# Optimization experiments

Hardware: AMD Instinct MI355X
Metric: run time of the kernel (lower is better)

Reference implementation:

```python
import jax, jax.numpy as jnp
import numpy as np

N_NODES = 100000
N_EDGES = 3200000
D_IN = 256
D_OUT = 128
LN_EPS = 1e-5


def setup_inputs() -> dict:
    key = jax.random.key(0)
    ks = jax.random.split(key, 6)
    stdv = 1.0 / np.sqrt(D_OUT)
    x = jax.random.normal(ks[0], (N_NODES, D_IN), dtype=jnp.float32)
    weight = jax.random.uniform(ks[1], (D_IN, D_OUT), minval=-stdv, maxval=stdv, dtype=jnp.float32)
    bias = jnp.zeros((D_OUT,), dtype=jnp.float32)
    res_w = jax.random.normal(ks[2], (D_IN, D_OUT), dtype=jnp.float32) * 0.05
    res_b = jnp.zeros((D_OUT,), dtype=jnp.float32)
    ln_gamma = jnp.ones((D_OUT,), dtype=jnp.float32)
    ln_beta = jnp.zeros((D_OUT,), dtype=jnp.float32)
    edge_weight = jax.random.uniform(ks[3], (N_EDGES,), dtype=jnp.float32)
    edge_index = jax.random.randint(ks[4], (2, N_EDGES), 0, N_NODES, dtype=jnp.int32)
    return {"x": x, "weight": weight, "bias": bias, "res_w": res_w, "res_b": res_b,
            "ln_gamma": ln_gamma, "ln_beta": ln_beta,
            "edge_weight": edge_weight, "edge_index": edge_index}


def reference(x, weight, bias, res_w, res_b, ln_gamma, ln_beta, edge_weight, edge_index):
    # dense projection: [N, D_IN] @ [D_IN, D_OUT]
    support = x @ weight
    # spmm: out[dst] += w_e * support[src]  (weighted COO aggregation)
    src, dst = edge_index[0], edge_index[1]
    msg = support[src] * edge_weight[:, None]          # [E, D_OUT]
    out = jax.ops.segment_sum(msg, dst, num_segments=N_NODES)
    # fused bias + activated residual branch
    out = out + bias + jax.nn.relu(x @ res_w + res_b)
    # layernorm over feature dim
    mu = jnp.mean(out, axis=-1, keepdims=True)
    var = jnp.mean(jnp.square(out - mu), axis=-1, keepdims=True)
    out = (out - mu) * jax.lax.rsqrt(var + LN_EPS) * ln_gamma + ln_beta
    return out
```

## Files before the change

### kernel.cpp

```cpp
#include <hip/hip_runtime.h>
#include <hip/hip_bf16.h>

#define D_IN 256
#define D_OUT 128
#define LN_EPS 1e-5f
#define NBUCK 256
#define NCHUNK 256

typedef short bf16x8 __attribute__((ext_vector_type(8)));
typedef float f32x4 __attribute__((ext_vector_type(4)));
typedef unsigned short ushort_t;

__device__ __forceinline__ float b2f(ushort_t u) {
    union { unsigned int i; float f; } v; v.i = (unsigned int)u << 16; return v.f;
}
__device__ __forceinline__ ushort_t f2b(float f) {
    __hip_bfloat16 h = __float2bfloat16(f);
    return *reinterpret_cast<ushort_t*>(&h);
}

__global__ void k_transpose(const float* __restrict__ w, const float* __restrict__ rw,
                            ushort_t* __restrict__ wt) {
    int idx = blockIdx.x * 256 + threadIdx.x;
    int n = idx >> 8, k = idx & 255;
    float v = (n < 128) ? w[k * 128 + n] : rw[k * 128 + (n - 128)];
    wt[idx] = f2b(v);
}

__launch_bounds__(256)
__global__ void k_gemm(const float* __restrict__ x, const ushort_t* __restrict__ wt,
                       const float* __restrict__ bias, const float* __restrict__ res_b,
                       ushort_t* __restrict__ support, float* __restrict__ out, int n_nodes) {
    __shared__ ushort_t As[64 * 40];
    __shared__ ushort_t Bs[256 * 40];

    const int tid = threadIdx.x;
    const int m0 = blockIdx.x * 64;
    const int wv = tid >> 6, lane = tid & 63;
    const int lm = lane & 15, quad = lane >> 4;
    const int mh = wv >> 1;
    const int nh = wv & 1;

    f32x4 acc[2][8];
#pragma unroll
    for (int i = 0; i < 2; i++)
#pragma unroll
        for (int j = 0; j < 8; j++) acc[i][j] = 0.0f;

    const int arow = tid >> 2, aseg = tid & 3;
    const bool arow_ok = (m0 + arow) < n_nodes;
    const float* xrow = x + (long)(m0 + arow) * D_IN + aseg * 8;

    for (int kc = 0; kc < 8; kc++) {
        __syncthreads();
        {
            bf16x8 av = {0, 0, 0, 0, 0, 0, 0, 0};
            if (arow_ok) {
                f32x4 p0 = *(const f32x4*)(xrow + kc * 32);
                f32x4 p1 = *(const f32x4*)(xrow + kc * 32 + 4);
#pragma unroll
                for (int j = 0; j < 4; j++) { av[j] = (short)f2b(p0[j]); av[4 + j] = (short)f2b(p1[j]); }
            }
            *(bf16x8*)(&As[arow * 40 + aseg * 8]) = av;
        }
#pragma unroll
        for (int i = 0; i < 4; i++) {
            int n = (tid >> 2) + i * 64;
            bf16x8 v = *(const bf16x8*)(wt + n * 256 + kc * 32 + aseg * 8);
            *(bf16x8*)(&Bs[n * 40 + aseg * 8]) = v;
        }
        __syncthreads();

        bf16x8 afr0 = *(const bf16x8*)(&As[(mh * 32 + lm) * 40 + quad * 8]);
        bf16x8 afr1 = *(const bf16x8*)(&As[(mh * 32 + 16 + lm) * 40 + quad * 8]);
#pragma unroll
        for (int nt = 0; nt < 8; nt++) {
            bf16x8 bfr = *(const bf16x8*)(&Bs[(nh * 128 + nt * 16 + lm) * 40 + quad * 8]);
            acc[0][nt] = __builtin_amdgcn_mfma_f32_16x16x32_bf16(afr0, bfr, acc[0][nt], 0, 0, 0);
            acc[1][nt] = __builtin_amdgcn_mfma_f32_16x16x32_bf16(afr1, bfr, acc[1][nt], 0, 0, 0);
        }
    }

#pragma unroll
    for (int i = 0; i < 2; i++) {
#pragma unroll
        for (int nt = 0; nt < 8; nt++) {
            int col = nh * 128 + nt * 16 + lm;
#pragma unroll
            for (int r = 0; r < 4; r++) {
                int node = m0 + mh * 32 + i * 16 + quad * 4 + r;
                if (node >= n_nodes) continue;
                float v = acc[i][nt][r];
                if (col < 128) {
                    support[(long)node * 128 + col] = f2b(v);
                } else {
                    int c2 = col - 128;
                    float t = v + res_b[c2];
                    t = t > 0.0f ? t : 0.0f;
                    out[(long)node * 128 + c2] = t + bias[c2];
                }
            }
        }
    }
}

__launch_bounds__(256)
__global__ void k_count(const int* __restrict__ ei, int* __restrict__ cntmat, int E, int chunk) {
    __shared__ int h[NBUCK];
    int c = blockIdx.x, t = threadIdx.x;
    h[t] = 0;
    __syncthreads();
    int lo = c * chunk, hi = min(lo + chunk, E);
    for (int e = lo + t; e < hi; e += 256)
        atomicAdd(&h[(unsigned)ei[E + e] >> 9], 1);
    __syncthreads();
    cntmat[t * NCHUNK + c] = h[t];
}

__launch_bounds__(256)
__global__ void k_scan1(int* __restrict__ cntmat, int* __restrict__ rowsum) {
    __shared__ int sh[256];
    int b = blockIdx.x, t = threadIdx.x;
    int v = cntmat[b * NCHUNK + t];
    sh[t] = v;
    __syncthreads();
    for (int off = 1; off < 256; off <<= 1) {
        int x = sh[t]; int add = (t >= off) ? sh[t - off] : 0;
        __syncthreads(); sh[t] = x + add; __syncthreads();
    }
    cntmat[b * NCHUNK + t] = sh[t] - v;
    if (t == 255) rowsum[b] = sh[255];
}

__launch_bounds__(256)
__global__ void k_scan2(const int* __restrict__ rowsum, int* __restrict__ bucket_base,
                        int* __restrict__ offs, int n_nodes, int E) {
    __shared__ int sh[256];
    int t = threadIdx.x;
    int v = rowsum[t];
    sh[t] = v;
    __syncthreads();
    for (int off = 1; off < 256; off <<= 1) {
        int x = sh[t]; int add = (t >= off) ? sh[t - off] : 0;
        __syncthreads(); sh[t] = x + add; __syncthreads();
    }
    bucket_base[t] = sh[t] - v;
    if (t == 255) bucket_base[256] = sh[255];
    if (t == 0) offs[n_nodes] = E;
}

__launch_bounds__(256)
__global__ void k_part(const int* __restrict__ ei, const float* __restrict__ ew,
                       const int* __restrict__ cntmat, const int* __restrict__ bucket_base,
                       int* __restrict__ pk, ushort_t* __restrict__ pw, int E, int chunk) {
    __shared__ int cur[NBUCK];
    int c = blockIdx.x, t = threadIdx.x;
    cur[t] = bucket_base[t] + cntmat[t * NCHUNK + c];
    __syncthreads();
    int lo = c * chunk, hi = min(lo + chunk, E);
    for (int e = lo + t; e < hi; e += 256) {
        int src = ei[e];
        int dst = ei[E + e];
        float w = ew[e];
        int b = (unsigned)dst >> 9;
        int pos = atomicAdd(&cur[b], 1);
        pk[pos] = src | ((dst & 511) << 17);
        pw[pos] = f2b(w);
    }
}

__launch_bounds__(256)
__global__ void k_build(const int* __restrict__ pk, const ushort_t* __restrict__ pw,
                        const int* __restrict__ bucket_base, int* __restrict__ sk,
                        ushort_t* __restrict__ sw, int* __restrict__ offs, int n_nodes) {
    __shared__ int h[512];
    __shared__ int psum[256];
    int b = blockIdx.x, t = threadIdx.x;
    int start = bucket_base[b], end = bucket_base[b + 1];
    h[t] = 0; h[t + 256] = 0;
    __syncthreads();
    for (int i = start + t; i < end; i += 256)
        atomicAdd(&h[(unsigned)pk[i] >> 17], 1);
    __syncthreads();
    int h0 = h[2 * t], h1 = h[2 * t + 1];
    int p = h0 + h1;
    psum[t] = p;
    __syncthreads();
    for (int off = 1; off < 256; off <<= 1) {
        int x = psum[t]; int add = (t >= off) ? psum[t - off] : 0;
        __syncthreads(); psum[t] = x + add; __syncthreads();
    }
    int e0 = psum[t] - p;
    int e1 = e0 + h0;
    h[2 * t] = e0; h[2 * t + 1] = e1;
    int node0 = b * 512 + 2 * t;
    if (node0 < n_nodes) offs[node0] = start + e0;
    if (node0 + 1 < n_nodes) offs[node0 + 1] = start + e1;
    __syncthreads();
    for (int i = start + t; i < end; i += 256) {
        int key = pk[i];
        int dl = (unsigned)key >> 17;
        int pos = start + atomicAdd(&h[dl], 1);
        sk[pos] = key;
        sw[pos] = pw[i];
    }
}

__launch_bounds__(256)
__global__ void k_agg_ln(const ushort_t* __restrict__ support, const int* __restrict__ offs,
                         const int* __restrict__ sk, const ushort_t* __restrict__ sw,
                         const float* __restrict__ gamma, const float* __restrict__ beta,
                         float* __restrict__ out, int n_nodes) {
    int gw = (int)((blockIdx.x * blockDim.x + threadIdx.x) >> 6);
    int lane = threadIdx.x & 63;
    int nw = (int)((gridDim.x * blockDim.x) >> 6);
    float g0 = gamma[lane * 2], g1 = gamma[lane * 2 + 1];
    float b0 = beta[lane * 2], b1 = beta[lane * 2 + 1];

    for (int node = gw; node < n_nodes; node += nw) {
        int start = offs[node], end = offs[node + 1];
        float ax = 0.0f, ay = 0.0f;
        for (int base = start; base < end; base += 64) {
            int n = end - base; if (n > 64) n = 64;
            int key = 0, wbits = 0;
            if (lane < n) {
                key = sk[base + lane];
                wbits = (int)sw[base + lane];
            }
            int j = 0;
            for (; j + 4 <= n; j += 4) {
                int s0 = __builtin_amdgcn_readlane(key, j + 0) & 131071;
                int s1 = __builtin_amdgcn_readlane(key, j + 1) & 131071;
                int s2 = __builtin_amdgcn_readlane(key, j + 2) & 131071;
                int s3 = __builtin_amdgcn_readlane(key, j + 3) & 131071;
                float w0 = b2f((ushort_t)__builtin_amdgcn_readlane(wbits, j + 0));
                float w1 = b2f((ushort_t)__builtin_amdgcn_readlane(wbits, j + 1));
                float w2 = b2f((ushort_t)__builtin_amdgcn_readlane(wbits, j + 2));
                float w3 = b2f((ushort_t)__builtin_amdgcn_readlane(wbits, j + 3));
                unsigned int v0 = *(const unsigned int*)(support + (long)s0 * 128 + lane * 2);
                unsigned int v1 = *(const unsigned int*)(support + (long)s1 * 128 + lane * 2);
                unsigned int v2 = *(const unsigned int*)(support + (long)s2 * 128 + lane * 2);
                unsigned int v3 = *(const unsigned int*)(support + (long)s3 * 128 + lane * 2);
                ax += w0 * b2f((ushort_t)(v0 & 0xffffu)) + w1 * b2f((ushort_t)(v1 & 0xffffu))
                    + w2 * b2f((ushort_t)(v2 & 0xffffu)) + w3 * b2f((ushort_t)(v3 & 0xffffu));
                ay += w0 * b2f((ushort_t)(v0 >> 16)) + w1 * b2f((ushort_t)(v1 >> 16))
                    + w2 * b2f((ushort_t)(v2 >> 16)) + w3 * b2f((ushort_t)(v3 >> 16));
            }
            for (; j < n; j++) {
                int sj = __builtin_amdgcn_readlane(key, j) & 131071;
                float wj = b2f((ushort_t)__builtin_amdgcn_readlane(wbits, j));
                unsigned int v = *(const unsigned int*)(support + (long)sj * 128 + lane * 2);
                ax += wj * b2f((ushort_t)(v & 0xffffu));
                ay += wj * b2f((ushort_t)(v >> 16));
            }
        }
        float2 r = *(const float2*)(out + (long)node * 128 + lane * 2);
        float tx = ax + r.x, ty = ay + r.y;
        float s = tx + ty;
        float ss = tx * tx + ty * ty;
#pragma unroll
        for (int off = 1; off < 64; off <<= 1) {
            s += __shfl_xor(s, off, 64);
            ss += __shfl_xor(ss, off, 64);
        }
        float mean = s * (1.0f / 128.0f);
        float var = ss * (1.0f / 128.0f) - mean * mean;
        float rstd = rsqrtf(var + LN_EPS);
        float2 o;
        o.x = (tx - mean) * rstd * g0 + b0;
        o.y = (ty - mean) * rstd * g1 + b1;
        *(float2*)(out + (long)node * 128 + lane * 2) = o;
    }
}

extern "C" void kernel_launch(void* const* d_in, const int* in_sizes, int n_in,
                              void* d_out, int out_size, void* d_ws, size_t ws_size,
                              hipStream_t stream) {
    const float* x      = (const float*)d_in[0];
    const float* weight = (const float*)d_in[1];
    const float* bias   = (const float*)d_in[2];
    const float* res_w  = (const float*)d_in[3];
    const float* res_b  = (const float*)d_in[4];
    const float* gamma  = (const float*)d_in[5];
    const float* beta   = (const float*)d_in[6];
    const float* ew     = (const float*)d_in[7];
    const int*   ei     = (const int*)d_in[8];

    const int E = in_sizes[7];
    const int n_nodes = in_sizes[0] / D_IN;
    const int chunk = (E + NCHUNK - 1) / NCHUNK;
    float* out = (float*)d_out;

    char* ws = (char*)d_ws;
    size_t off = 0;
    auto alloc = [&](size_t bytes) { void* p = ws + off; off = (off + bytes + 255) & ~(size_t)255; return p; };
    ushort_t* wt      = (ushort_t*)alloc(256 * 256 * 2);
    ushort_t* support = (ushort_t*)alloc((size_t)n_nodes * 128 * 2);
    int* cntmat       = (int*)alloc((size_t)NBUCK * NCHUNK * 4);
    int* rowsum       = (int*)alloc(NBUCK * 4);
    int* bucket_base  = (int*)alloc((NBUCK + 1) * 4);
    int* offs         = (int*)alloc((size_t)(n_nodes + 1) * 4);
    int* pk           = (int*)alloc((size_t)E * 4);
    ushort_t* pw      = (ushort_t*)alloc((size_t)E * 2);
    int* sk           = (int*)alloc((size_t)E * 4);
    ushort_t* sw      = (ushort_t*)alloc((size_t)E * 2);

    k_transpose<<<256, 256, 0, stream>>>(weight, res_w, wt);
    k_gemm<<<(n_nodes + 63) / 64, 256, 0, stream>>>(x, wt, bias, res_b, support, out, n_nodes);
    k_count<<<NCHUNK, 256, 0, stream>>>(ei, cntmat, E, chunk);
    k_scan1<<<NBUCK, 256, 0, stream>>>(cntmat, rowsum);
    k_scan2<<<1, 256, 0, stream>>>(rowsum, bucket_base, offs, n_nodes, E);
    k_part<<<NCHUNK, 256, 0, stream>>>(ei, ew, cntmat, bucket_base, pk, pw, E, chunk);
    k_build<<<NBUCK, 256, 0, stream>>>(pk, pw, bucket_base, sk, sw, offs, n_nodes);
    k_agg_ln<<<4096, 256, 0, stream>>>(support, offs, sk, sw, gamma, beta, out, n_nodes);
}
```

Before: 504.5 us.

## Replace two-level bucket sort with global-atomic CSR build and fp32 edge records

Replaces the two-pass bucket partition (count/scan/part/build with LDS atomics) with a direct per-node histogram using global atomics, a three-stage prefix scan, and a global-atomic scatter into CSR order. Edge records become int2 holding the src index and the fp32 weight, so weights are no longer rounded to bf16 and the key masking goes away. The aggregation loop is unrolled to 8 gathers per step. This trades two passes over the edges for one, at the cost of heavy global atomic contention on 3.2M edges and 8-byte records, which raises the memory traffic of the scatter and gather phases.

```diff
diff --git a/kernel.cpp b/kernel.cpp
--- a/kernel.cpp
+++ b/kernel.cpp
@@ -4,8 +4,6 @@
 #define D_IN 256
 #define D_OUT 128
 #define LN_EPS 1e-5f
-#define NBUCK 256
-#define NCHUNK 256
 
 typedef short bf16x8 __attribute__((ext_vector_type(8)));
 typedef float f32x4 __attribute__((ext_vector_type(4)));
@@ -20,11 +18,14 @@
 }
 
 __global__ void k_transpose(const float* __restrict__ w, const float* __restrict__ rw,
-                            ushort_t* __restrict__ wt) {
+                            ushort_t* __restrict__ wt, int* __restrict__ ncnt, int n_nodes) {
     int idx = blockIdx.x * 256 + threadIdx.x;
     int n = idx >> 8, k = idx & 255;
     float v = (n < 128) ? w[k * 128 + n] : rw[k * 128 + (n - 128)];
     wt[idx] = f2b(v);
+    if (idx < n_nodes) ncnt[idx] = 0;
+    int i2 = idx + 65536;
+    if (i2 < n_nodes) ncnt[i2] = 0;
 }
 
 __launch_bounds__(256)
@@ -105,110 +106,83 @@
 }
 
 __launch_bounds__(256)
-__global__ void k_count(const int* __restrict__ ei, int* __restrict__ cntmat, int E, int chunk) {
-    __shared__ int h[NBUCK];
-    int c = blockIdx.x, t = threadIdx.x;
-    h[t] = 0;
-    __syncthreads();
-    int lo = c * chunk, hi = min(lo + chunk, E);
-    for (int e = lo + t; e < hi; e += 256)
-        atomicAdd(&h[(unsigned)ei[E + e] >> 9], 1);
-    __syncthreads();
-    cntmat[t * NCHUNK + c] = h[t];
-}
-
-__launch_bounds__(256)
-__global__ void k_scan1(int* __restrict__ cntmat, int* __restrict__ rowsum) {
+__global__ void k_hist(const int* __restrict__ ei, int* __restrict__ ncnt, int E) {
+    int i = blockIdx.x * blockDim.x + threadIdx.x;
+    int st = gridDim.x * blockDim.x;
+    for (int e = i; e < E; e += st)
+        atomicAdd(&ncnt[ei[E + e]], 1);
+}
+
+__launch_bounds__(256)
+__global__ void k_scanA(const int* __restrict__ ncnt, int* __restrict__ poff,
+                        int* __restrict__ bsum, int n) {
     __shared__ int sh[256];
     int b = blockIdx.x, t = threadIdx.x;
-    int v = cntmat[b * NCHUNK + t];
+    int e0 = b * 1024 + t * 4;
+    int v0 = (e0 + 0 < n) ? ncnt[e0 + 0] : 0;
+    int v1 = (e0 + 1 < n) ? ncnt[e0 + 1] : 0;
+    int v2 = (e0 + 2 < n) ? ncnt[e0 + 2] : 0;
+    int v3 = (e0 + 3 < n) ? ncnt[e0 + 3] : 0;
+    int s3 = v0 + v1 + v2 + v3;
+    sh[t] = s3;
+    __syncthreads();
+    for (int off = 1; off < 256; off <<= 1) {
+        int x = sh[t]; int add = (t >= off) ? sh[t - off] : 0;
+        __syncthreads(); sh[t] = x + add; __syncthreads();
+    }
+    int excl = sh[t] - s3;
+    if (e0 + 0 < n) poff[e0 + 0] = excl;
+    if (e0 + 1 < n) poff[e0 + 1] = excl + v0;
+    if (e0 + 2 < n) poff[e0 + 2] = excl + v0 + v1;
+    if (e0 + 3 < n) poff[e0 + 3] = excl + v0 + v1 + v2;
+    if (t == 255) bsum[b] = sh[255];
+}
+
+__launch_bounds__(256)
+__global__ void k_scanB(const int* __restrict__ bsum, int* __restrict__ bbase,
+                        int* __restrict__ offs, int nb, int n, int E) {
+    __shared__ int sh[256];
+    int t = threadIdx.x;
+    int v = (t < nb) ? bsum[t] : 0;
     sh[t] = v;
     __syncthreads();
     for (int off = 1; off < 256; off <<= 1) {
         int x = sh[t]; int add = (t >= off) ? sh[t - off] : 0;
         __syncthreads(); sh[t] = x + add; __syncthreads();
     }
-    cntmat[b * NCHUNK + t] = sh[t] - v;
-    if (t == 255) rowsum[b] = sh[255];
-}
-
-__launch_bounds__(256)
-__global__ void k_scan2(const int* __restrict__ rowsum, int* __restrict__ bucket_base,
-                        int* __restrict__ offs, int n_nodes, int E) {
-    __shared__ int sh[256];
-    int t = threadIdx.x;
-    int v = rowsum[t];
-    sh[t] = v;
-    __syncthreads();
-    for (int off = 1; off < 256; off <<= 1) {
-        int x = sh[t]; int add = (t >= off) ? sh[t - off] : 0;
-        __syncthreads(); sh[t] = x + add; __syncthreads();
-    }
-    bucket_base[t] = sh[t] - v;
-    if (t == 255) bucket_base[256] = sh[255];
-    if (t == 0) offs[n_nodes] = E;
-}
-
-__launch_bounds__(256)
-__global__ void k_part(const int* __restrict__ ei, const float* __restrict__ ew,
-                       const int* __restrict__ cntmat, const int* __restrict__ bucket_base,
-                       int* __restrict__ pk, ushort_t* __restrict__ pw, int E, int chunk) {
-    __shared__ int cur[NBUCK];
-    int c = blockIdx.x, t = threadIdx.x;
-    cur[t] = bucket_base[t] + cntmat[t * NCHUNK + c];
-    __syncthreads();
-    int lo = c * chunk, hi = min(lo + chunk, E);
-    for (int e = lo + t; e < hi; e += 256) {
+    bbase[t] = sh[t] - v;
+    if (t == 0) offs[n] = E;
+}
+
+__launch_bounds__(256)
+__global__ void k_scanC(const int* __restrict__ poff, const int* __restrict__ bbase,
+                        int* __restrict__ offs, int* __restrict__ ncur, int n) {
+    int i = blockIdx.x * 256 + threadIdx.x;
+    if (i < n) {
+        int o = poff[i] + bbase[i >> 10];
+        offs[i] = o;
+        ncur[i] = o;
+    }
+}
+
+__launch_bounds__(256)
+__global__ void k_scatter(const int* __restrict__ ei, const float* __restrict__ ew,
+                          int* __restrict__ ncur, int2* __restrict__ recs, int E) {
+    int i = blockIdx.x * blockDim.x + threadIdx.x;
+    int st = gridDim.x * blockDim.x;
+    for (int e = i; e < E; e += st) {
         int src = ei[e];
         int dst = ei[E + e];
         float w = ew[e];
-        int b = (unsigned)dst >> 9;
-        int pos = atomicAdd(&cur[b], 1);
-        pk[pos] = src | ((dst & 511) << 17);
-        pw[pos] = f2b(w);
-    }
-}
-
-__launch_bounds__(256)
-__global__ void k_build(const int* __restrict__ pk, const ushort_t* __restrict__ pw,
-                        const int* __restrict__ bucket_base, int* __restrict__ sk,
-                        ushort_t* __restrict__ sw, int* __restrict__ offs, int n_nodes) {
-    __shared__ int h[512];
-    __shared__ int psum[256];
-    int b = blockIdx.x, t = threadIdx.x;
-    int start = bucket_base[b], end = bucket_base[b + 1];
-    h[t] = 0; h[t + 256] = 0;
-    __syncthreads();
-    for (int i = start + t; i < end; i += 256)
-        atomicAdd(&h[(unsigned)pk[i] >> 17], 1);
-    __syncthreads();
-    int h0 = h[2 * t], h1 = h[2 * t + 1];
-    int p = h0 + h1;
-    psum[t] = p;
-    __syncthreads();
-    for (int off = 1; off < 256; off <<= 1) {
-        int x = psum[t]; int add = (t >= off) ? psum[t - off] : 0;
-        __syncthreads(); psum[t] = x + add; __syncthreads();
-    }
-    int e0 = psum[t] - p;
-    int e1 = e0 + h0;
-    h[2 * t] = e0; h[2 * t + 1] = e1;
-    int node0 = b * 512 + 2 * t;
-    if (node0 < n_nodes) offs[node0] = start + e0;
-    if (node0 + 1 < n_nodes) offs[node0 + 1] = start + e1;
-    __syncthreads();
-    for (int i = start + t; i < end; i += 256) {
-        int key = pk[i];
-        int dl = (unsigned)key >> 17;
-        int pos = start + atomicAdd(&h[dl], 1);
-        sk[pos] = key;
-        sw[pos] = pw[i];
+        int pos = atomicAdd(&ncur[dst], 1);
+        int2 r; r.x = src; r.y = __float_as_int(w);
+        recs[pos] = r;
     }
 }
 
 __launch_bounds__(256)
 __global__ void k_agg_ln(const ushort_t* __restrict__ support, const int* __restrict__ offs,
-                         const int* __restrict__ sk, const ushort_t* __restrict__ sw,
+                         const int2* __restrict__ recs,
                          const float* __restrict__ gamma, const float* __restrict__ beta,
                          float* __restrict__ out, int n_nodes) {
     int gw = (int)((blockIdx.x * blockDim.x + threadIdx.x) >> 6);
@@ -216,40 +190,37 @@
     int nw = (int)((gridDim.x * blockDim.x) >> 6);
     float g0 = gamma[lane * 2], g1 = gamma[lane * 2 + 1];
     float b0 = beta[lane * 2], b1 = beta[lane * 2 + 1];
+    const ushort_t* sup_lane = support + lane * 2;
 
     for (int node = gw; node < n_nodes; node += nw) {
         int start = offs[node], end = offs[node + 1];
         float ax = 0.0f, ay = 0.0f;
         for (int base = start; base < end; base += 64) {
             int n = end - base; if (n > 64) n = 64;
-            int key = 0, wbits = 0;
+            int key = 0, wb = 0;
             if (lane < n) {
-                key = sk[base + lane];
-                wbits = (int)sw[base + lane];
+                int2 r = recs[base + lane];
+                key = r.x; wb = r.y;
             }
             int j = 0;
-            for (; j + 4 <= n; j += 4) {
-                int s0 = __builtin_amdgcn_readlane(key, j + 0) & 131071;
-                int s1 = __builtin_amdgcn_readlane(key, j + 1) & 131071;
-                int s2 = __builtin_amdgcn_readlane(key, j + 2) & 131071;
-                int s3 = __builtin_amdgcn_readlane(key, j + 3) & 131071;
-                float w0 = b2f((ushort_t)__builtin_amdgcn_readlane(wbits, j + 0));
-                float w1 = b2f((ushort_t)__builtin_amdgcn_readlane(wbits, j + 1));
-                float w2 = b2f((ushort_t)__builtin_amdgcn_readlane(wbits, j + 2));
-                float w3 = b2f((ushort_t)__builtin_amdgcn_readlane(wbits, j + 3));
-                unsigned int v0 = *(const unsigned int*)(support + (long)s0 * 128 + lane * 2);
-                unsigned int v1 = *(const unsigned int*)(support + (long)s1 * 128 + lane * 2);
-                unsigned int v2 = *(const unsigned int*)(support + (long)s2 * 128 + lane * 2);
-                unsigned int v3 = *(const unsigned int*)(support + (long)s3 * 128 + lane * 2);
-                ax += w0 * b2f((ushort_t)(v0 & 0xffffu)) + w1 * b2f((ushort_t)(v1 & 0xffffu))
-                    + w2 * b2f((ushort_t)(v2 & 0xffffu)) + w3 * b2f((ushort_t)(v3 & 0xffffu));
-                ay += w0 * b2f((ushort_t)(v0 >> 16)) + w1 * b2f((ushort_t)(v1 >> 16))
-                    + w2 * b2f((ushort_t)(v2 >> 16)) + w3 * b2f((ushort_t)(v3 >> 16));
+            for (; j + 8 <= n; j += 8) {
+                unsigned int v[8]; float w[8];
+#pragma unroll
+                for (int u = 0; u < 8; u++) {
+                    int s = __builtin_amdgcn_readlane(key, j + u);
+                    w[u] = __int_as_float(__builtin_amdgcn_readlane(wb, j + u));
+                    v[u] = *(const unsigned int*)(sup_lane + (long)s * 128);
+                }
+#pragma unroll
+                for (int u = 0; u < 8; u++) {
+                    ax += w[u] * b2f((ushort_t)(v[u] & 0xffffu));
+                    ay += w[u] * b2f((ushort_t)(v[u] >> 16));
+                }
             }
             for (; j < n; j++) {
-                int sj = __builtin_amdgcn_readlane(key, j) & 131071;
-                float wj = b2f((ushort_t)__builtin_amdgcn_readlane(wbits, j));
-                unsigned int v = *(const unsigned int*)(support + (long)sj * 128 + lane * 2);
+                int s = __builtin_amdgcn_readlane(key, j);
+                float wj = __int_as_float(__builtin_amdgcn_readlane(wb, j));
+                unsigned int v = *(const unsigned int*)(sup_lane + (long)s * 128);
                 ax += wj * b2f((ushort_t)(v & 0xffffu));
                 ay += wj * b2f((ushort_t)(v >> 16));
             }
@@ -288,7 +259,6 @@
 
     const int E = in_sizes[7];
     const int n_nodes = in_sizes[0] / D_IN;
-    const int chunk = (E + NCHUNK - 1) / NCHUNK;
     float* out = (float*)d_out;
 
     char* ws = (char*)d_ws;
@@ -296,21 +266,22 @@
     auto alloc = [&](size_t bytes) { void* p = ws + off; off = (off + bytes + 255) & ~(size_t)255; return p; };
     ushort_t* wt      = (ushort_t*)alloc(256 * 256 * 2);
     ushort_t* support = (ushort_t*)alloc((size_t)n_nodes * 128 * 2);
-    int* cntmat       = (int*)alloc((size_t)NBUCK * NCHUNK * 4);
-    int* rowsum       = (int*)alloc(NBUCK * 4);
-    int* bucket_base  = (int*)alloc((NBUCK + 1) * 4);
+    int* ncnt         = (int*)alloc((size_t)n_nodes * 4);
+    int* poff         = (int*)alloc((size_t)n_nodes * 4);
+    int* bsum         = (int*)alloc(256 * 4);
+    int* bbase        = (int*)alloc(256 * 4);
     int* offs         = (int*)alloc((size_t)(n_nodes + 1) * 4);
-    int* pk           = (int*)alloc((size_t)E * 4);
-    ushort_t* pw      = (ushort_t*)alloc((size_t)E * 2);
-    int* sk           = (int*)alloc((size_t)E * 4);
-    ushort_t* sw      = (ushort_t*)alloc((size_t)E * 2);
-
-    k_transpose<<<256, 256, 0, stream>>>(weight, res_w, wt);
+    int* ncur         = (int*)alloc((size_t)n_nodes * 4);
+    int2* recs        = (int2*)alloc((size_t)E * 8);
+
+    int nbA = (n_nodes + 1023) / 1024;
+
+    k_transpose<<<256, 256, 0, stream>>>(weight, res_w, wt, ncnt, n_nodes);
     k_gemm<<<(n_nodes + 63) / 64, 256, 0, stream>>>(x, wt, bias, res_b, support, out, n_nodes);
-    k_count<<<NCHUNK, 256, 0, stream>>>(ei, cntmat, E, chunk);
-    k_scan1<<<NBUCK, 256, 0, stream>>>(cntmat, rowsum);
-    k_scan2<<<1, 256, 0, stream>>>(rowsum, bucket_base, offs, n_nodes, E);
-    k_part<<<NCHUNK, 256, 0, stream>>>(ei, ew, cntmat, bucket_base, pk, pw, E, chunk);
-    k_build<<<NBUCK, 256, 0, stream>>>(pk, pw, bucket_base, sk, sw, offs, n_nodes);
-    k_agg_ln<<<4096, 256, 0, stream>>>(support, offs, sk, sw, gamma, beta, out, n_nodes);
-}
+    k_hist<<<2048, 256, 0, stream>>>(ei, ncnt, E);
+    k_scanA<<<nbA, 256, 0, stream>>>(ncnt, poff, bsum, n_nodes);
+    k_scanB<<<1, 256, 0, stream>>>(bsum, bbase, offs, nbA, n_nodes, E);
+    k_scanC<<<(n_nodes + 255) / 256, 256, 0, stream>>>(poff, bbase, offs, ncur, n_nodes);
+    k_scatter<<<2048, 256, 0, stream>>>(ei, ew, ncur, recs, E);
+    k_agg_ln<<<4096, 256, 0, stream>>>(support, offs, recs, gamma, beta, out, n_nodes);
+}
```

Result: slower. 738.8 us (+46.4%).
